# Performance work log

Measured on AMD Instinct MI355X. Metric: run time of the kernel, lower is better.

## Reference

```python
import jax, jax.numpy as jnp
import numpy as np

EPS = 1e-08

def _safe_sqrt(x):
    # sqrt with zero (not nan) gradient at 0, matching torch's guarded cdist/norm backward
    pos = x > 0
    return jnp.where(pos, jnp.sqrt(jnp.where(pos, x, 1.0)), 0.0)

def setup_inputs() -> dict:
    key = jax.random.key(0)
    k1, k2, k3 = jax.random.split(key, 3)
    B, D, K = 1000000, 64, 64
    latent_z = jax.random.normal(k1, (B, D), dtype=jnp.float32)
    cluster_assignments = jax.random.uniform(k2, (B, K), dtype=jnp.float32)
    cluster_centers = jax.random.normal(k3, (K, D), dtype=jnp.float32)
    return {"latent_z": latent_z, "cluster_assignments": cluster_assignments, "cluster_centers": cluster_centers}

def reference(latent_z, cluster_assignments, cluster_centers):
    K = cluster_centers.shape[0]
    balance_weight, separation_weight, compactness_weight = 0.1, 0.1, 0.1

    # --- balance: KL(uniform || mean assignment probs), reduction='sum' ---
    cluster_probs = jnp.mean(cluster_assignments, axis=0)              # [K]
    uniform = 1.0 / K
    balance_loss = jnp.sum(uniform * (jnp.log(uniform) - jnp.log(cluster_probs + EPS)))

    # --- separation: mean pairwise off-diagonal center distance (negated) ---
    diff = cluster_centers[:, None, :] - cluster_centers[None, :, :]   # [K,K,D]
    sq = jnp.sum(diff * diff, axis=-1)                                 # [K,K]
    center_distances = _safe_sqrt(sq)
    mask = ~jnp.eye(K, dtype=bool)
    separation_loss = -jnp.sum(jnp.where(mask, center_distances, 0.0)) / (K * (K - 1))

    # --- compactness: mean distance to own center per cluster, averaged over non-empty clusters ---
    hard = jnp.argmax(cluster_assignments, axis=1)                     # [B] int
    d = latent_z - cluster_centers[hard]                               # [B,D]
    dist = _safe_sqrt(jnp.sum(d * d, axis=1))                          # [B]
    per_cluster_sum = jax.ops.segment_sum(dist, hard, num_segments=K)  # [K]
    counts = jax.ops.segment_sum(jnp.ones_like(dist), hard, num_segments=K)
    nonempty = counts > 0
    per_cluster_mean = per_cluster_sum / jnp.maximum(counts, 1.0)
    n_nonempty = jnp.sum(nonempty.astype(jnp.float32))
    compactness_loss = jnp.sum(jnp.where(nonempty, per_cluster_mean, 0.0)) / jnp.maximum(n_nonempty, 1.0)

    auxiliary_loss = (balance_weight * balance_loss
                      + separation_weight * separation_loss
                      + compactness_weight * compactness_loss)
    cluster_balance = jnp.std(cluster_probs, ddof=1)  # torch std is unbiased
    return (auxiliary_loss, balance_loss, separation_loss, compactness_loss, cluster_balance)
```

## Files before the change

kernel.cpp:

```cpp
#include <hip/hip_runtime.h>

#define KC 64
#define DD 64


__global__ __launch_bounds__(256, 8) void aux_main(
    const float* __restrict__ z,
    const float* __restrict__ assign,
    const float* __restrict__ centers,
    float* __restrict__ ws, int B)
{
    __shared__ float s_c[KC * DD];
    __shared__ float s_colsum[KC];
    __shared__ float s_dist[KC];
    __shared__ float s_cnt[KC];

    const int tid = threadIdx.x;

    {
        const float4* c4 = (const float4*)centers;
        float4* s4 = (float4*)s_c;
        for (int i = tid; i < KC * DD / 4; i += 256) s4[i] = c4[i];
    }
    if (tid < KC) { s_colsum[tid] = 0.f; s_dist[tid] = 0.f; s_cnt[tid] = 0.f; }
    __syncthreads();

    const int wave   = tid >> 6;
    const int lane   = tid & 63;
    const int subrow = lane >> 4;
    const int sub    = lane & 15;

    const int gw   = blockIdx.x * 4 + wave;
    const int nw   = gridDim.x * 4;
    const int ngrp = (B + 3) >> 2;

    float cs0 = 0.f, cs1 = 0.f, cs2 = 0.f, cs3 = 0.f;

    for (int g = gw; g < ngrp; g += nw) {
        int r = g * 4 + subrow;
        if (r < B) {
            size_t off = (size_t)r * DD + sub * 4;

            float4 a = *(const float4*)(assign + off);
            cs0 += a.x; cs1 += a.y; cs2 += a.z; cs3 += a.w;

            float m = a.x; int mi = 0;
            if (a.y > m) { m = a.y; mi = 1; }
            if (a.z > m) { m = a.z; mi = 2; }
            if (a.w > m) { m = a.w; mi = 3; }
            mi += sub * 4;

            #pragma unroll
            for (int d = 1; d < 16; d <<= 1) {
                float om  = __shfl_xor(m, d, 16);
                int   omi = __shfl_xor(mi, d, 16);
                if (om > m || (om == m && omi < mi)) { m = om; mi = omi; }
            }
            const int hard = mi;

            float4 zv = *(const float4*)(z + off);
            const float* cp = &s_c[hard * DD + sub * 4];
            float d0 = zv.x - cp[0], d1 = zv.y - cp[1];
            float d2 = zv.z - cp[2], d3 = zv.w - cp[3];
            float ss = d0*d0 + d1*d1 + d2*d2 + d3*d3;

            #pragma unroll
            for (int d = 1; d < 16; d <<= 1) ss += __shfl_xor(ss, d, 16);

            if (sub == 0) {
                atomicAdd(&s_dist[hard], ss > 0.f ? sqrtf(ss) : 0.f);
                atomicAdd(&s_cnt[hard], 1.f);
            }
        }
    }

    atomicAdd(&s_colsum[sub * 4 + 0], cs0);
    atomicAdd(&s_colsum[sub * 4 + 1], cs1);
    atomicAdd(&s_colsum[sub * 4 + 2], cs2);
    atomicAdd(&s_colsum[sub * 4 + 3], cs3);
    __syncthreads();

    if (tid < KC) {
        atomicAdd(&ws[tid],       s_colsum[tid]);
        atomicAdd(&ws[64 + tid],  s_dist[tid]);
        atomicAdd(&ws[128 + tid], s_cnt[tid]);
    }
}

__global__ void aux_sep(const float* __restrict__ centers, float* __restrict__ ws)
{
    __shared__ float rowi[DD];
    const int i = blockIdx.x;
    const int j = threadIdx.x;

    if (j < 16) ((float4*)rowi)[j] = ((const float4*)(centers + (size_t)i * DD))[j];
    __syncthreads();

    float ss = 0.f;
    const float4* cj = (const float4*)(centers + (size_t)j * DD);
    #pragma unroll
    for (int q = 0; q < 16; q++) {
        float4 u = cj[q];
        float e0 = u.x - rowi[q*4+0], e1 = u.y - rowi[q*4+1];
        float e2 = u.z - rowi[q*4+2], e3 = u.w - rowi[q*4+3];
        ss += e0*e0 + e1*e1 + e2*e2 + e3*e3;
    }
    float dist = (i != j && ss > 0.f) ? sqrtf(ss) : 0.f;

    #pragma unroll
    for (int d = 1; d < 64; d <<= 1) dist += __shfl_xor(dist, d, 64);
    if (j == 0) atomicAdd(&ws[192], dist);
}

__global__ void aux_fin(const float* __restrict__ ws, float* __restrict__ out, int B)
{
    const int k = threadIdx.x;
    const float uni = 1.0f / 64.0f;

    float p   = ws[k] / (float)B;
    float bal = uni * (logf(uni) - logf(p + 1e-8f));

    float cnt = ws[128 + k];
    float ne  = cnt > 0.f ? 1.f : 0.f;
    float pcm = ne * (ws[64 + k] / fmaxf(cnt, 1.f));
    float ps  = p;

    #pragma unroll
    for (int d = 1; d < 64; d <<= 1) {
        bal += __shfl_xor(bal, d, 64);
        ne  += __shfl_xor(ne,  d, 64);
        pcm += __shfl_xor(pcm, d, 64);
        ps  += __shfl_xor(ps,  d, 64);
    }

    float comp = pcm / fmaxf(ne, 1.f);
    float pm   = ps * (1.0f / 64.0f);
    float dv   = (p - pm) * (p - pm);
    #pragma unroll
    for (int d = 1; d < 64; d <<= 1) dv += __shfl_xor(dv, d, 64);
    float stdv = sqrtf(dv / 63.0f);

    float sep = -ws[192] / (64.0f * 63.0f);

    if (k == 0) {
        out[0] = 0.1f * bal + 0.1f * sep + 0.1f * comp;
        out[1] = bal;
        out[2] = sep;
        out[3] = comp;
        out[4] = stdv;
    }
}

extern "C" void kernel_launch(void* const* d_in, const int* in_sizes, int n_in,
                              void* d_out, int out_size, void* d_ws, size_t ws_size,
                              hipStream_t stream) {
    const float* z       = (const float*)d_in[0];
    const float* assign  = (const float*)d_in[1];
    const float* centers = (const float*)d_in[2];
    float* ws = (float*)d_ws;
    const int B = in_sizes[0] / DD;

    hipMemsetAsync(d_ws, 0, 1024, stream);
    aux_sep<<<64, 64, 0, stream>>>(centers, ws);
    aux_main<<<2048, 256, 0, stream>>>(z, assign, centers, ws, B);
    aux_fin<<<1, 64, 0, stream>>>(ws, (float*)d_out, B);
}
```

Before: 520.1 us.

## Process four-lane groups per row with more loads in flight and swizzled centers

```diff
diff --git a/kernel.cpp b/kernel.cpp
--- a/kernel.cpp
+++ b/kernel.cpp
@@ -4,13 +4,13 @@
 #define DD 64
 
 
-__global__ __launch_bounds__(256, 8) void aux_main(
+__global__ __launch_bounds__(256, 6) void aux_main(
     const float* __restrict__ z,
     const float* __restrict__ assign,
     const float* __restrict__ centers,
     float* __restrict__ ws, int B)
 {
-    __shared__ float s_c[KC * DD];
+    __shared__ float4 s_c4[KC * DD / 4];
     __shared__ float s_colsum[KC];
     __shared__ float s_dist[KC];
     __shared__ float s_cnt[KC];
@@ -19,65 +19,104 @@
 
     {
         const float4* c4 = (const float4*)centers;
-        float4* s4 = (float4*)s_c;
-        for (int i = tid; i < KC * DD / 4; i += 256) s4[i] = c4[i];
+        for (int i = tid; i < KC * DD / 4; i += 256) {
+            int k = i >> 4, c = i & 15;
+            s_c4[(k << 4) | (c ^ (k & 7))] = c4[i];
+        }
     }
     if (tid < KC) { s_colsum[tid] = 0.f; s_dist[tid] = 0.f; s_cnt[tid] = 0.f; }
     __syncthreads();
 
-    const int wave   = tid >> 6;
-    const int lane   = tid & 63;
-    const int subrow = lane >> 4;
-    const int sub    = lane & 15;
+    const int wave = tid >> 6;
+    const int lane = tid & 63;
+    const int row4 = lane >> 2;
+    const int qd   = lane & 3;
 
     const int gw   = blockIdx.x * 4 + wave;
     const int nw   = gridDim.x * 4;
-    const int ngrp = (B + 3) >> 2;
-
-    float cs0 = 0.f, cs1 = 0.f, cs2 = 0.f, cs3 = 0.f;
+    const int ngrp = (B + 15) >> 4;
+
+    float4 cs0 = {0,0,0,0}, cs1 = {0,0,0,0}, cs2 = {0,0,0,0}, cs3 = {0,0,0,0};
 
     for (int g = gw; g < ngrp; g += nw) {
-        int r = g * 4 + subrow;
+        const int r = g * 16 + row4;
         if (r < B) {
-            size_t off = (size_t)r * DD + sub * 4;
-
-            float4 a = *(const float4*)(assign + off);
-            cs0 += a.x; cs1 += a.y; cs2 += a.z; cs3 += a.w;
-
-            float m = a.x; int mi = 0;
-            if (a.y > m) { m = a.y; mi = 1; }
-            if (a.z > m) { m = a.z; mi = 2; }
-            if (a.w > m) { m = a.w; mi = 3; }
-            mi += sub * 4;
+            const float4* ap = (const float4*)assign + ((size_t)r << 4) + qd;
+            const float4* zp = (const float4*)z      + ((size_t)r << 4) + qd;
+            float4 a0 = ap[0], a1 = ap[4], a2 = ap[8],  a3 = ap[12];
+            float4 z0 = zp[0], z1 = zp[4], z2 = zp[8],  z3 = zp[12];
+
+            cs0.x += a0.x; cs0.y += a0.y; cs0.z += a0.z; cs0.w += a0.w;
+            cs1.x += a1.x; cs1.y += a1.y; cs1.z += a1.z; cs1.w += a1.w;
+            cs2.x += a2.x; cs2.y += a2.y; cs2.z += a2.z; cs2.w += a2.w;
+            cs3.x += a3.x; cs3.y += a3.y; cs3.z += a3.z; cs3.w += a3.w;
+
+            const int cb0 = qd * 4;
+            float m = a0.x; int mi = cb0;
+            #define CAND(v, c) if ((v) > m) { m = (v); mi = (c); }
+            CAND(a0.y, cb0 + 1)  CAND(a0.z, cb0 + 2)  CAND(a0.w, cb0 + 3)
+            CAND(a1.x, 16 + cb0) CAND(a1.y, 17 + cb0) CAND(a1.z, 18 + cb0) CAND(a1.w, 19 + cb0)
+            CAND(a2.x, 32 + cb0) CAND(a2.y, 33 + cb0) CAND(a2.z, 34 + cb0) CAND(a2.w, 35 + cb0)
+            CAND(a3.x, 48 + cb0) CAND(a3.y, 49 + cb0) CAND(a3.z, 50 + cb0) CAND(a3.w, 51 + cb0)
+            #undef CAND
 
             #pragma unroll
-            for (int d = 1; d < 16; d <<= 1) {
-                float om  = __shfl_xor(m, d, 16);
-                int   omi = __shfl_xor(mi, d, 16);
+            for (int d = 1; d < 4; d <<= 1) {
+                float om  = __shfl_xor(m, d, 4);
+                int   omi = __shfl_xor(mi, d, 4);
                 if (om > m || (om == m && omi < mi)) { m = om; mi = omi; }
             }
             const int hard = mi;
 
-            float4 zv = *(const float4*)(z + off);
-            const float* cp = &s_c[hard * DD + sub * 4];
-            float d0 = zv.x - cp[0], d1 = zv.y - cp[1];
-            float d2 = zv.z - cp[2], d3 = zv.w - cp[3];
-            float ss = d0*d0 + d1*d1 + d2*d2 + d3*d3;
-
-            #pragma unroll
-            for (int d = 1; d < 16; d <<= 1) ss += __shfl_xor(ss, d, 16);
-
-            if (sub == 0) {
+            const float4* cb = s_c4 + (hard << 4);
+            const int sw = hard & 7;
+            float4 c0 = cb[(qd +  0) ^ sw];
+            float4 c1 = cb[(qd +  4) ^ sw];
+            float4 c2 = cb[(qd +  8) ^ sw];
+            float4 c3 = cb[(qd + 12) ^ sw];
+
+            float d0, ss = 0.f;
+            d0 = z0.x - c0.x; ss += d0 * d0;  d0 = z0.y - c0.y; ss += d0 * d0;
+            d0 = z0.z - c0.z; ss += d0 * d0;  d0 = z0.w - c0.w; ss += d0 * d0;
+            d0 = z1.x - c1.x; ss += d0 * d0;  d0 = z1.y - c1.y; ss += d0 * d0;
+            d0 = z1.z - c1.z; ss += d0 * d0;  d0 = z1.w - c1.w; ss += d0 * d0;
+            d0 = z2.x - c2.x; ss += d0 * d0;  d0 = z2.y - c2.y; ss += d0 * d0;
+            d0 = z2.z - c2.z; ss += d0 * d0;  d0 = z2.w - c2.w; ss += d0 * d0;
+            d0 = z3.x - c3.x; ss += d0 * d0;  d0 = z3.y - c3.y; ss += d0 * d0;
+            d0 = z3.z - c3.z; ss += d0 * d0;  d0 = z3.w - c3.w; ss += d0 * d0;
+
+            ss += __shfl_xor(ss, 1, 4);
+            ss += __shfl_xor(ss, 2, 4);
+
+            if (qd == 0) {
                 atomicAdd(&s_dist[hard], ss > 0.f ? sqrtf(ss) : 0.f);
                 atomicAdd(&s_cnt[hard], 1.f);
             }
         }
     }
 
-    atomicAdd(&s_colsum[sub * 4 + 0], cs0);
-    atomicAdd(&s_colsum[sub * 4 + 1], cs1);
-    atomicAdd(&s_colsum[sub * 4 + 2], cs2);
-    atomicAdd(&s_colsum[sub * 4 + 3], cs3);
+    #pragma unroll
+    for (int d = 4; d < 64; d <<= 1) {
+        cs0.x += __shfl_xor(cs0.x, d); cs0.y += __shfl_xor(cs0.y, d);
+        cs0.z += __shfl_xor(cs0.z, d); cs0.w += __shfl_xor(cs0.w, d);
+        cs1.x += __shfl_xor(cs1.x, d); cs1.y += __shfl_xor(cs1.y, d);
+        cs1.z += __shfl_xor(cs1.z, d); cs1.w += __shfl_xor(cs1.w, d);
+        cs2.x += __shfl_xor(cs2.x, d); cs2.y += __shfl_xor(cs2.y, d);
+        cs2.z += __shfl_xor(cs2.z, d); cs2.w += __shfl_xor(cs2.w, d);
+        cs3.x += __shfl_xor(cs3.x, d); cs3.y += __shfl_xor(cs3.y, d);
+        cs3.z += __shfl_xor(cs3.z, d); cs3.w += __shfl_xor(cs3.w, d);
+    }
+    if (lane < 4) {
+        const int b = lane * 4;
+        atomicAdd(&s_colsum[ 0 + b + 0], cs0.x); atomicAdd(&s_colsum[ 0 + b + 1], cs0.y);
+        atomicAdd(&s_colsum[ 0 + b + 2], cs0.z); atomicAdd(&s_colsum[ 0 + b + 3], cs0.w);
+        atomicAdd(&s_colsum[16 + b + 0], cs1.x); atomicAdd(&s_colsum[16 + b + 1], cs1.y);
+        atomicAdd(&s_colsum[16 + b + 2], cs1.z); atomicAdd(&s_colsum[16 + b + 3], cs1.w);
+        atomicAdd(&s_colsum[32 + b + 0], cs2.x); atomicAdd(&s_colsum[32 + b + 1], cs2.y);
+        atomicAdd(&s_colsum[32 + b + 2], cs2.z); atomicAdd(&s_colsum[32 + b + 3], cs2.w);
+        atomicAdd(&s_colsum[48 + b + 0], cs3.x); atomicAdd(&s_colsum[48 + b + 1], cs3.y);
+        atomicAdd(&s_colsum[48 + b + 2], cs3.z); atomicAdd(&s_colsum[48 + b + 3], cs3.w);
+    }
     __syncthreads();
 
     if (tid < KC) {
@@ -162,6 +201,6 @@
 
     hipMemsetAsync(d_ws, 0, 1024, stream);
     aux_sep<<<64, 64, 0, stream>>>(centers, ws);
-    aux_main<<<2048, 256, 0, stream>>>(z, assign, centers, ws, B);
+    aux_main<<<1536, 256, 0, stream>>>(z, assign, centers, ws, B);
     aux_fin<<<1, 64, 0, stream>>>(ws, (float*)d_out, B);
 }
```

After: 495.0 us. 4.8% less time.
